# Kernel optimization log

Hardware: AMD Instinct MI355X
Metric: run time of the kernel (lower is better)

## Reference

```python
import jax, jax.numpy as jnp
import numpy as np

N_NODES = 50000
N_EDGES = 800000
IN_CH = 256
H1, D1 = 4, 64   # layer 1: 4 heads x 64 -> 256
H2, D2 = 1, 64   # output layer: 1 head x 64
NEG_SLOPE = 0.2  # DGL GATConv default


def _leaky_relu(x):
    return jnp.where(x >= 0, x, NEG_SLOPE * x)


def gat_conv(h, src, dst, W, attn_l, attn_r, bias, res_W, num_heads, out_feats, apply_elu):
    """DGL GATConv (eval mode, feat_drop=attn_drop=0).
    h: (N, F_in); src/dst: (E,) edge endpoints (edge u->v aggregates at v).
    W: (F_in, H*D); attn_l/attn_r: (H, D); bias: (H*D,); res_W: (F_in, H*D) or None.
    Returns (N, H, D).
    """
    N = h.shape[0]
    ft = (h @ W).reshape(N, num_heads, out_feats)            # (N,H,D)
    el = jnp.sum(ft * attn_l, axis=-1)                        # (N,H)
    er = jnp.sum(ft * attn_r, axis=-1)                        # (N,H)
    e = _leaky_relu(el[src] + er[dst])                        # (E,H)
    # segment softmax over incoming edges of each dst node
    emax = jax.ops.segment_max(e, dst, num_segments=N)        # (N,H)
    emax = jax.lax.stop_gradient(emax)
    ee = jnp.exp(e - emax[dst])                               # (E,H)
    denom = jax.ops.segment_sum(ee, dst, num_segments=N)      # (N,H)
    a = ee / denom[dst]                                       # (E,H)
    msg = ft[src] * a[:, :, None]                             # (E,H,D)
    rst = jax.ops.segment_sum(msg, dst, num_segments=N)       # (N,H,D)
    if res_W is not None:
        rst = rst + (h @ res_W).reshape(N, num_heads, out_feats)
    rst = rst + bias.reshape(num_heads, out_feats)
    if apply_elu:
        rst = jax.nn.elu(rst)
    return rst


def setup_inputs() -> dict:
    key = jax.random.key(0)
    ks = jax.random.split(key, 12)
    feat = jax.random.normal(ks[0], (N_NODES, IN_CH), dtype=jnp.float32)
    src = jax.random.randint(ks[1], (N_EDGES,), 0, N_NODES)
    dst = jax.random.randint(ks[2], (N_EDGES,), 0, N_NODES)
    s = 0.1
    W1 = jax.random.normal(ks[3], (IN_CH, H1 * D1), dtype=jnp.float32) * s
    al1 = jax.random.normal(ks[4], (H1, D1), dtype=jnp.float32) * s
    ar1 = jax.random.normal(ks[5], (H1, D1), dtype=jnp.float32) * s
    b1 = jnp.zeros((H1 * D1,), dtype=jnp.float32)
    W2 = jax.random.normal(ks[6], (H1 * D1, H2 * D2), dtype=jnp.float32) * s
    al2 = jax.random.normal(ks[7], (H2, D2), dtype=jnp.float32) * s
    ar2 = jax.random.normal(ks[8], (H2, D2), dtype=jnp.float32) * s
    b2 = jnp.zeros((H2 * D2,), dtype=jnp.float32)
    resW2 = jax.random.normal(ks[9], (H1 * D1, H2 * D2), dtype=jnp.float32) * s
    return {"feat": feat, "src": src, "dst": dst,
            "W1": W1, "al1": al1, "ar1": ar1, "b1": b1,
            "W2": W2, "al2": al2, "ar2": ar2, "b2": b2, "resW2": resW2}


def reference(feat, src, dst, W1, al1, ar1, b1, W2, al2, ar2, b2, resW2):
    # Layer 1: 4 heads, ELU, no residual (first DGL layer built without residual)
    h = gat_conv(feat, src, dst, W1, al1, ar1, b1, None, H1, D1, True)
    h = h.reshape(N_NODES, H1 * D1)  # flatten(1)
    # Layer 2: 1 head, residual (linear res_fc since 256 != 64), no activation
    h = gat_conv(h, src, dst, W2, al2, ar2, b2, resW2, H2, D2, False)
    return h.mean(axis=1)  # mean over output heads -> (N, out_channels)
```

## Files before the change

### kernel.cpp

```cpp
#include <hip/hip_runtime.h>
#include <math.h>

#define N_NODES 50000
#define N_EDGES 800000
#define ELL_W 64
#define CNT_STRIDE 16

#define E_SPLIT 400000
#define CONV_BLKS 1792
#define SCAT_BLKS 512

typedef __attribute__((ext_vector_type(8))) short bf16x8;
typedef __attribute__((ext_vector_type(4))) float f32x4;
typedef __attribute__((ext_vector_type(2))) float f32x2;

__device__ __forceinline__ float leaky(float x) { return x >= 0.f ? x : 0.2f * x; }
__device__ __forceinline__ unsigned short f2bf(float f) {
  unsigned u = __float_as_uint(f);
  return (unsigned short)((u + 0x7fffu + ((u >> 16) & 1u)) >> 16);
}
__device__ __forceinline__ float bflo(unsigned u) { return __uint_as_float(u << 16); }
__device__ __forceinline__ float bfhi(unsigned u) { return __uint_as_float(u & 0xffff0000u); }
__device__ __forceinline__ unsigned pack2(float a, float b) {
  return (unsigned)f2bf(a) | ((unsigned)f2bf(b) << 16);
}

__device__ __forceinline__ void scat4(const int* __restrict__ src, const int* __restrict__ dst,
                                      int* __restrict__ cnt, unsigned short* __restrict__ ell,
                                      int e) {
  int4 d4 = *(const int4*)(dst + e);
  int4 s4 = *(const int4*)(src + e);
  int sl;
  sl = atomicAdd(cnt + d4.x * CNT_STRIDE, 1);
  if (sl < ELL_W) __builtin_nontemporal_store((unsigned short)s4.x, ell + d4.x * ELL_W + sl);
  sl = atomicAdd(cnt + d4.y * CNT_STRIDE, 1);
  if (sl < ELL_W) __builtin_nontemporal_store((unsigned short)s4.y, ell + d4.y * ELL_W + sl);
  sl = atomicAdd(cnt + d4.z * CNT_STRIDE, 1);
  if (sl < ELL_W) __builtin_nontemporal_store((unsigned short)s4.z, ell + d4.z * ELL_W + sl);
  sl = atomicAdd(cnt + d4.w * CNT_STRIDE, 1);
  if (sl < ELL_W) __builtin_nontemporal_store((unsigned short)s4.w, ell + d4.w * ELL_W + sl);
}

__launch_bounds__(256)
__global__ void prep_k(const float* __restrict__ feat, const float* __restrict__ W1,
                       const float* __restrict__ W2, const float* __restrict__ resW2,
                       short* __restrict__ featb, short* __restrict__ Wt1,
                       short* __restrict__ Wt2, const int* __restrict__ src,
                       const int* __restrict__ dst, int* __restrict__ cnt,
                       unsigned short* __restrict__ ell) {
  if (blockIdx.x < SCAT_BLKS) {
    const int gtid = blockIdx.x * 256 + threadIdx.x;
    const int gsz = SCAT_BLKS * 256;
    for (int q = gtid; q < E_SPLIT / 4; q += gsz) scat4(src, dst, cnt, ell, q * 4);
    return;
  }
  const int gtid = (blockIdx.x - SCAT_BLKS) * 256 + threadIdx.x;
  const int gsz = CONV_BLKS * 256;
  for (int idx = gtid; idx < 256 * 256; idx += gsz) {
    int n = idx >> 8, k = idx & 255;
    Wt1[idx] = (short)f2bf(W1[(size_t)k * 256 + n]);
  }
  for (int idx = gtid; idx < 128 * 256; idx += gsz) {
    int n = idx >> 8, k = idx & 255;
    float v = (n < 64) ? W2[(size_t)k * 64 + n] : resW2[(size_t)k * 64 + (n - 64)];
    Wt2[idx] = (short)f2bf(v);
  }
  const float4* f4 = (const float4*)feat;
  uint2* fb2 = (uint2*)featb;
  for (int idx = gtid; idx < N_NODES * 64; idx += gsz) {
    float4 f = f4[idx];
    uint2 o;
    o.x = pack2(f.x, f.y);
    o.y = pack2(f.z, f.w);
    fb2[idx] = o;
  }
}

template <int MODE, bool SCAT>
__launch_bounds__(256)
__global__ void mfma_gemm_k(const short* __restrict__ A, const short* __restrict__ Bt,
                            const float* __restrict__ bias, const float* __restrict__ al,
                            const float* __restrict__ ar, float* __restrict__ elp,
                            float* __restrict__ erp, short* __restrict__ Cb,
                            float* __restrict__ Cf, const int* __restrict__ src,
                            const int* __restrict__ dst, int* __restrict__ cnt,
                            unsigned short* __restrict__ ell, int M, int K, int N) {
  constexpr int EPI_COLS = (MODE == 0) ? 136 : 72;
  union SharedU {
    struct { short As[4][128][8]; short Bs[4][128][8]; } ab;
    short epi[128 * EPI_COLS];
  };
  __shared__ SharedU sh;

  if (SCAT && blockIdx.y == 0) {
    const int gtid = blockIdx.x * 256 + threadIdx.x;
    const int gsz = gridDim.x * 256;
    for (int q = gtid; q < (N_EDGES - E_SPLIT) / 4; q += gsz)
      scat4(src, dst, cnt, ell, E_SPLIT + q * 4);
    return;
  }
  const int tid = threadIdx.x;
  const int bm0 = blockIdx.x * 128;
  const int bn0 = (SCAT ? ((int)blockIdx.y - 1) : (int)blockIdx.y) * 128;
  const int wave = tid >> 6, lane = tid & 63;
  const int wm = (wave & 1) * 64, wn = (wave >> 1) * 64;
  const int q = lane >> 4, r16 = lane & 15;
  const int srow = tid >> 1, sk = (tid & 1) * 16, sq = (tid & 1) * 2;
  f32x4 acc[4][4] = {};

  for (int k0 = 0; k0 < K; k0 += 32) {
    {
      uint4 v0 = {0, 0, 0, 0}, v1 = {0, 0, 0, 0};
      if (bm0 + srow < M) {
        const uint4* p = (const uint4*)(A + (size_t)(bm0 + srow) * K + k0 + sk);
        v0 = p[0];
        v1 = p[1];
      }
      *(uint4*)&sh.ab.As[sq][srow][0] = v0;
      *(uint4*)&sh.ab.As[sq + 1][srow][0] = v1;
    }
    {
      const uint4* p = (const uint4*)(Bt + (size_t)(bn0 + srow) * K + k0 + sk);
      *(uint4*)&sh.ab.Bs[sq][srow][0] = p[0];
      *(uint4*)&sh.ab.Bs[sq + 1][srow][0] = p[1];
    }
    __syncthreads();
    bf16x8 af[4], bfr[4];
#pragma unroll
    for (int i = 0; i < 4; ++i) af[i] = *(const bf16x8*)&sh.ab.As[q][wm + i * 16 + r16][0];
#pragma unroll
    for (int j = 0; j < 4; ++j) bfr[j] = *(const bf16x8*)&sh.ab.Bs[q][wn + j * 16 + r16][0];
#pragma unroll
    for (int i = 0; i < 4; ++i)
#pragma unroll
      for (int j = 0; j < 4; ++j)
        acc[i][j] = __builtin_amdgcn_mfma_f32_16x16x32_bf16(af[i], bfr[j], acc[i][j], 0, 0, 0);
    __syncthreads();
  }

  if (MODE == 0 || wn == 0) {
    const int head = (bn0 + wn) >> 6;
    float alv[4], arv[4];
#pragma unroll
    for (int j = 0; j < 4; ++j) {
      alv[j] = al[((MODE == 0) ? head * 64 : 0) + j * 16 + r16];
      arv[j] = ar[((MODE == 0) ? head * 64 : 0) + j * 16 + r16];
    }
#pragma unroll
    for (int i = 0; i < 4; ++i) {
#pragma unroll
      for (int reg = 0; reg < 4; ++reg) {
        float dl = acc[i][0][reg] * alv[0] + acc[i][1][reg] * alv[1] +
                   acc[i][2][reg] * alv[2] + acc[i][3][reg] * alv[3];
        float dr = acc[i][0][reg] * arv[0] + acc[i][1][reg] * arv[1] +
                   acc[i][2][reg] * arv[2] + acc[i][3][reg] * arv[3];
#pragma unroll
        for (int mm = 1; mm < 16; mm <<= 1) {
          dl += __shfl_xor(dl, mm);
          dr += __shfl_xor(dr, mm);
        }
        int row_g = bm0 + wm + i * 16 + q * 4 + reg;
        if (r16 == 0 && row_g < M) {
          if (MODE == 0) {
            elp[(size_t)row_g * 4 + head] = dl;
            erp[(size_t)row_g * 4 + head] = dr;
          } else {
            elp[row_g] = dl;
            erp[row_g] = dr;
          }
        }
      }
    }
  }

  if (MODE == 0) {
#pragma unroll
    for (int i = 0; i < 4; ++i)
#pragma unroll
      for (int reg = 0; reg < 4; ++reg) {
        int row = wm + i * 16 + q * 4 + reg;
#pragma unroll
        for (int j = 0; j < 4; ++j)
          sh.epi[row * EPI_COLS + wn + j * 16 + r16] = (short)f2bf(acc[i][j][reg]);
      }
    __syncthreads();
#pragma unroll
    for (int k = 0; k < 8; ++k) {
      int c = k * 256 + tid;
      int row = c >> 4, cc = c & 15;
      int row_g = bm0 + row;
      if (row_g < M) {
        uint4 v = *(const uint4*)&sh.epi[row * EPI_COLS + cc * 8];
        *(uint4*)(Cb + (size_t)row_g * N + bn0 + cc * 8) = v;
      }
    }
  } else {
    if (wn == 0) {
#pragma unroll
      for (int i = 0; i < 4; ++i)
#pragma unroll
        for (int reg = 0; reg < 4; ++reg) {
          int row = wm + i * 16 + q * 4 + reg;
#pragma unroll
          for (int j = 0; j < 4; ++j)
            sh.epi[row * EPI_COLS + j * 16 + r16] = (short)f2bf(acc[i][j][reg]);
        }
    } else {
#pragma unroll
      for (int i = 0; i < 4; ++i)
#pragma unroll
        for (int reg = 0; reg < 4; ++reg) {
          int row_g = bm0 + wm + i * 16 + q * 4 + reg;
          if (row_g >= M) continue;
#pragma unroll
          for (int j = 0; j < 4; ++j) {
            int col = j * 16 + r16;
            Cf[(size_t)row_g * 64 + col] = acc[i][j][reg] + bias[col];
          }
        }
    }
    __syncthreads();
#pragma unroll
    for (int k = 0; k < 4; ++k) {
      int c = k * 256 + tid;
      int row = c >> 3, cc = c & 7;
      int row_g = bm0 + row;
      if (row_g < M) {
        uint4 v = *(const uint4*)&sh.epi[row * EPI_COLS + cc * 8];
        *(uint4*)(Cb + (size_t)row_g * 64 + cc * 8) = v;
      }
    }
  }
}

__launch_bounds__(256)
__global__ void agg1_k(const unsigned short* __restrict__ ell, const int* __restrict__ cnt,
                       const float* __restrict__ el, const float* __restrict__ er,
                       const short* __restrict__ ft, const float* __restrict__ bias,
                       short* __restrict__ h1) {
  __shared__ unsigned wofs[4][64];
  __shared__ float wval[4][4][64];
  const int nib = threadIdx.x >> 6;
  const int node = blockIdx.x * 4 + nib;
  const int lane = threadIdx.x & 63;
  if (node >= N_NODES) return;
  const int deg = min(cnt[node * CNT_STRIDE], ELL_W);
  const unsigned short* row = ell + node * ELL_W;

  {
    int s_raw = row[lane];
    bool val = lane < deg;
    int s0 = deg > 0 ? (int)row[0] : 0;
    int s_safe = val ? s_raw : s0;
    float4 el4 = *(const float4*)(el + (size_t)s_safe * 4);
    float4 er4 = *(const float4*)(er + (size_t)node * 4);
    float w0 = val ? __expf(leaky(el4.x + er4.x)) : 0.f;
    float w1 = val ? __expf(leaky(el4.y + er4.y)) : 0.f;
    float w2 = val ? __expf(leaky(el4.z + er4.z)) : 0.f;
    float w3 = val ? __expf(leaky(el4.w + er4.w)) : 0.f;
    float d0 = w0, d1 = w1, d2 = w2, d3 = w3;
#pragma unroll
    for (int m = 1; m < 64; m <<= 1) {
      d0 += __shfl_xor(d0, m);
      d1 += __shfl_xor(d1, m);
      d2 += __shfl_xor(d2, m);
      d3 += __shfl_xor(d3, m);
    }
    float i0 = deg > 0 ? 1.f / d0 : 0.f;
    float i1 = deg > 0 ? 1.f / d1 : 0.f;
    float i2 = deg > 0 ? 1.f / d2 : 0.f;
    float i3 = deg > 0 ? 1.f / d3 : 0.f;
    wofs[nib][lane] = (unsigned)s_safe * 512u;
    wval[nib][0][lane] = w0 * i0;
    wval[nib][1][lane] = w1 * i1;
    wval[nib][2][lane] = w2 * i2;
    wval[nib][3][lane] = w3 * i3;
  }

  const int half = lane >> 5, l5 = lane & 31, h = l5 >> 3;
  const char* ftb = (const char*)ft + l5 * 16;
  const float* wv = &wval[nib][h][0];
  const unsigned* wo = &wofs[nib][0];
  f32x2 acc2[4] = {};
  const int degR = (deg + 7) & ~7;
  for (int i = 0; i < degR; i += 8) {
    unsigned o[4];
    float w[4];
    uint4 u[4];
#pragma unroll
    for (int k = 0; k < 4; ++k) {
      int slot = i + k * 2 + half;
      o[k] = wo[slot];
      w[k] = wv[slot];
    }
#pragma unroll
    for (int k = 0; k < 4; ++k) u[k] = *(const uint4*)(ftb + o[k]);
#pragma unroll
    for (int k = 0; k < 4; ++k) {
      f32x2 w2 = {w[k], w[k]};
      f32x2 p0 = {bflo(u[k].x), bfhi(u[k].x)};
      f32x2 p1 = {bflo(u[k].y), bfhi(u[k].y)};
      f32x2 p2 = {bflo(u[k].z), bfhi(u[k].z)};
      f32x2 p3 = {bflo(u[k].w), bfhi(u[k].w)};
      acc2[0] += w2 * p0;
      acc2[1] += w2 * p1;
      acc2[2] += w2 * p2;
      acc2[3] += w2 * p3;
    }
  }
#pragma unroll
  for (int j = 0; j < 4; ++j) {
    acc2[j][0] += __shfl_xor(acc2[j][0], 32);
    acc2[j][1] += __shfl_xor(acc2[j][1], 32);
  }
  if (half == 0) {
    float4 b0 = *(const float4*)(bias + l5 * 8);
    float4 b1 = *(const float4*)(bias + l5 * 8 + 4);
    float v[8];
    v[0] = acc2[0][0] + b0.x;
    v[1] = acc2[0][1] + b0.y;
    v[2] = acc2[1][0] + b0.z;
    v[3] = acc2[1][1] + b0.w;
    v[4] = acc2[2][0] + b1.x;
    v[5] = acc2[2][1] + b1.y;
    v[6] = acc2[3][0] + b1.z;
    v[7] = acc2[3][1] + b1.w;
#pragma unroll
    for (int k = 0; k < 8; ++k) v[k] = v[k] > 0.f ? v[k] : expm1f(v[k]);
    uint4 o;
    o.x = pack2(v[0], v[1]);
    o.y = pack2(v[2], v[3]);
    o.z = pack2(v[4], v[5]);
    o.w = pack2(v[6], v[7]);
    *(uint4*)(h1 + (size_t)node * 256 + l5 * 8) = o;
  }
}

__launch_bounds__(256)
__global__ void agg2_k(const unsigned short* __restrict__ ell, const int* __restrict__ cnt,
                       const float* __restrict__ el, const float* __restrict__ er,
                       const short* __restrict__ ft, float* __restrict__ out) {
  __shared__ uint2 wsl[4][64];
  const int nib = threadIdx.x >> 6;
  const int node = blockIdx.x * 4 + nib;
  const int lane = threadIdx.x & 63;
  if (node >= N_NODES) return;
  const int deg = min(cnt[node * CNT_STRIDE], ELL_W);
  const unsigned short* row = ell + node * ELL_W;

  {
    int s_raw = row[lane];
    bool val = lane < deg;
    int s0 = deg > 0 ? (int)row[0] : 0;
    int s_safe = val ? s_raw : s0;
    float erd = er[node];
    float w = val ? __expf(leaky(el[s_safe] + erd)) : 0.f;
    float d = w;
#pragma unroll
    for (int m = 1; m < 64; m <<= 1) d += __shfl_xor(d, m);
    float inv = deg > 0 ? 1.f / d : 0.f;
    uint2 e;
    e.x = (unsigned)s_safe * 128u;
    e.y = __float_as_uint(w * inv);
    wsl[nib][lane] = e;
  }

  const int qtr = lane >> 4, l4 = lane & 15;
  const char* ftb = (const char*)ft + l4 * 8;
  f32x2 acc2[2] = {};
  const int degR = (deg + 7) & ~7;
  for (int i = 0; i < degR; i += 8) {
#pragma unroll
    for (int k = 0; k < 2; ++k) {
      int slot = i + k * 4 + qtr;
      uint2 e = wsl[nib][slot];
      uint2 u = *(const uint2*)(ftb + e.x);
      float w = __uint_as_float(e.y);
      f32x2 w2 = {w, w};
      f32x2 p0 = {bflo(u.x), bfhi(u.x)};
      f32x2 p1 = {bflo(u.y), bfhi(u.y)};
      acc2[0] += w2 * p0;
      acc2[1] += w2 * p1;
    }
  }
#pragma unroll
  for (int j = 0; j < 2; ++j) {
#pragma unroll
    for (int c = 0; c < 2; ++c) {
      acc2[j][c] += __shfl_xor(acc2[j][c], 16);
      acc2[j][c] += __shfl_xor(acc2[j][c], 32);
    }
  }
  if (lane < 16) {
    float4* po = (float4*)(out + (size_t)node * 64 + l4 * 4);
    float4 o = *po;
    o.x += acc2[0][0];
    o.y += acc2[0][1];
    o.z += acc2[1][0];
    o.w += acc2[1][1];
    *po = o;
  }
}

extern "C" void kernel_launch(void* const* d_in, const int* in_sizes, int n_in,
                              void* d_out, int out_size, void* d_ws, size_t ws_size,
                              hipStream_t stream) {
  const float* feat  = (const float*)d_in[0];
  const int*   src   = (const int*)d_in[1];
  const int*   dst   = (const int*)d_in[2];
  const float* W1    = (const float*)d_in[3];
  const float* al1   = (const float*)d_in[4];
  const float* ar1   = (const float*)d_in[5];
  const float* b1    = (const float*)d_in[6];
  const float* W2    = (const float*)d_in[7];
  const float* al2   = (const float*)d_in[8];
  const float* ar2   = (const float*)d_in[9];
  const float* b2    = (const float*)d_in[10];
  const float* resW2 = (const float*)d_in[11];
  float* out = (float*)d_out;

  char* p = (char*)d_ws;
  short* featb = (short*)p; p += (size_t)N_NODES * 256 * 2;
  short* ft1b = (short*)p; p += (size_t)N_NODES * 256 * 2;
  short* h1b  = (short*)p; p += (size_t)N_NODES * 256 * 2;
  short* ft2b = (short*)p; p += (size_t)N_NODES * 64 * 2;
  short* Wt1  = (short*)p; p += 256 * 256 * 2;
  short* Wt2  = (short*)p; p += 128 * 256 * 2;
  float* el1  = (float*)p; p += (size_t)N_NODES * 4 * 4;
  float* er1  = (float*)p; p += (size_t)N_NODES * 4 * 4;
  float* el2  = (float*)p; p += (size_t)N_NODES * 4;
  float* er2  = (float*)p; p += (size_t)N_NODES * 4;
  int* cnt    = (int*)p;   p += (size_t)N_NODES * CNT_STRIDE * 4;
  unsigned short* ell = (unsigned short*)p; p += (size_t)N_NODES * ELL_W * 2;

  hipMemsetAsync(cnt, 0, (size_t)N_NODES * CNT_STRIDE * sizeof(int), stream);

  dim3 blk(256);

  prep_k<<<SCAT_BLKS + CONV_BLKS, blk, 0, stream>>>(feat, W1, W2, resW2, featb, Wt1, Wt2,
                                                    src, dst, cnt, ell);

  mfma_gemm_k<0, true><<<dim3(391, 3), blk, 0, stream>>>(
      featb, Wt1, nullptr, al1, ar1, el1, er1, ft1b, nullptr,
      src, dst, cnt, ell, N_NODES, 256, 256);
  agg1_k<<<12500, blk, 0, stream>>>(ell, cnt, el1, er1, ft1b, b1, h1b);

  mfma_gemm_k<1, false><<<dim3(391, 1), blk, 0, stream>>>(
      h1b, Wt2, b2, al2, ar2, el2, er2, ft2b, out,
      nullptr, nullptr, nullptr, nullptr, N_NODES, 256, 128);
  agg2_k<<<12500, blk, 0, stream>>>(ell, cnt, el2, er2, ft2b, out);
}
```

Before: 275.7 us.

## Process two nodes per wave in aggregation kernels and widen edge-scatter grid

Both aggregation kernels now assign two destination nodes to each wavefront, interleaving their gathers to raise memory-level parallelism and halving the grid. Layer-1 softmax weights and offsets are packed into one shared array so a single LDS read yields both. The scatter work inside the first GEMM now runs one item per thread over two grid rows, and the prep kernel block split is rebalanced. The cost is more registers per thread and wasted work when the two nodes' degrees differ.

```diff
diff --git a/kernel.cpp b/kernel.cpp
--- a/kernel.cpp
+++ b/kernel.cpp
@@ -7,8 +7,8 @@
 #define CNT_STRIDE 16
 
 #define E_SPLIT 400000
-#define CONV_BLKS 1792
-#define SCAT_BLKS 512
+#define CONV_BLKS 1024
+#define SCAT_BLKS 1024
 
 typedef __attribute__((ext_vector_type(8))) short bf16x8;
 typedef __attribute__((ext_vector_type(4))) float f32x4;
@@ -92,16 +92,14 @@
   };
   __shared__ SharedU sh;
 
-  if (SCAT && blockIdx.y == 0) {
-    const int gtid = blockIdx.x * 256 + threadIdx.x;
-    const int gsz = gridDim.x * 256;
-    for (int q = gtid; q < (N_EDGES - E_SPLIT) / 4; q += gsz)
-      scat4(src, dst, cnt, ell, E_SPLIT + q * 4);
+  if (SCAT && blockIdx.y < 2) {
+    const int gtid = (blockIdx.y * gridDim.x + blockIdx.x) * 256 + threadIdx.x;
+    if (gtid < (N_EDGES - E_SPLIT) / 4) scat4(src, dst, cnt, ell, E_SPLIT + gtid * 4);
     return;
   }
   const int tid = threadIdx.x;
   const int bm0 = blockIdx.x * 128;
-  const int bn0 = (SCAT ? ((int)blockIdx.y - 1) : (int)blockIdx.y) * 128;
+  const int bn0 = (SCAT ? ((int)blockIdx.y - 2) : (int)blockIdx.y) * 128;
   const int wave = tid >> 6, lane = tid & 63;
   const int wm = (wave & 1) * 64, wn = (wave >> 1) * 64;
   const int q = lane >> 4, r16 = lane & 15;
@@ -233,171 +231,209 @@
   }
 }
 
+#define AGG1_FMA(ACC, U, W)                     \
+  {                                             \
+    f32x2 w2_ = {(W), (W)};                     \
+    ACC[0] += w2_ * (f32x2){bflo((U).x), bfhi((U).x)}; \
+    ACC[1] += w2_ * (f32x2){bflo((U).y), bfhi((U).y)}; \
+    ACC[2] += w2_ * (f32x2){bflo((U).z), bfhi((U).z)}; \
+    ACC[3] += w2_ * (f32x2){bflo((U).w), bfhi((U).w)}; \
+  }
+
 __launch_bounds__(256)
 __global__ void agg1_k(const unsigned short* __restrict__ ell, const int* __restrict__ cnt,
                        const float* __restrict__ el, const float* __restrict__ er,
                        const short* __restrict__ ft, const float* __restrict__ bias,
                        short* __restrict__ h1) {
-  __shared__ unsigned wofs[4][64];
-  __shared__ float wval[4][4][64];
-  const int nib = threadIdx.x >> 6;
-  const int node = blockIdx.x * 4 + nib;
+  __shared__ uint2 wmeta[4][2][64][4];
+  const int wv = threadIdx.x >> 6;
   const int lane = threadIdx.x & 63;
-  if (node >= N_NODES) return;
-  const int deg = min(cnt[node * CNT_STRIDE], ELL_W);
-  const unsigned short* row = ell + node * ELL_W;
+  const int nodeA = blockIdx.x * 8 + wv * 2;
+  const int nodeB = nodeA + 1;
+  const int degA = min(cnt[nodeA * CNT_STRIDE], ELL_W);
+  const int degB = min(cnt[nodeB * CNT_STRIDE], ELL_W);
+  const unsigned short* rowA = ell + nodeA * ELL_W;
+  const unsigned short* rowB = ell + nodeB * ELL_W;
 
   {
-    int s_raw = row[lane];
-    bool val = lane < deg;
-    int s0 = deg > 0 ? (int)row[0] : 0;
-    int s_safe = val ? s_raw : s0;
-    float4 el4 = *(const float4*)(el + (size_t)s_safe * 4);
-    float4 er4 = *(const float4*)(er + (size_t)node * 4);
-    float w0 = val ? __expf(leaky(el4.x + er4.x)) : 0.f;
-    float w1 = val ? __expf(leaky(el4.y + er4.y)) : 0.f;
-    float w2 = val ? __expf(leaky(el4.z + er4.z)) : 0.f;
-    float w3 = val ? __expf(leaky(el4.w + er4.w)) : 0.f;
-    float d0 = w0, d1 = w1, d2 = w2, d3 = w3;
+    int sA = lane < degA ? (int)rowA[lane] : (degA > 0 ? (int)rowA[0] : 0);
+    int sB = lane < degB ? (int)rowB[lane] : (degB > 0 ? (int)rowB[0] : 0);
+    float4 elA = *(const float4*)(el + (size_t)sA * 4);
+    float4 elB = *(const float4*)(el + (size_t)sB * 4);
+    float4 erA = *(const float4*)(er + (size_t)nodeA * 4);
+    float4 erB = *(const float4*)(er + (size_t)nodeB * 4);
+    float a0 = lane < degA ? __expf(leaky(elA.x + erA.x)) : 0.f;
+    float a1 = lane < degA ? __expf(leaky(elA.y + erA.y)) : 0.f;
+    float a2 = lane < degA ? __expf(leaky(elA.z + erA.z)) : 0.f;
+    float a3 = lane < degA ? __expf(leaky(elA.w + erA.w)) : 0.f;
+    float b0 = lane < degB ? __expf(leaky(elB.x + erB.x)) : 0.f;
+    float b1 = lane < degB ? __expf(leaky(elB.y + erB.y)) : 0.f;
+    float b2 = lane < degB ? __expf(leaky(elB.z + erB.z)) : 0.f;
+    float b3 = lane < degB ? __expf(leaky(elB.w + erB.w)) : 0.f;
+    float dA0 = a0, dA1 = a1, dA2 = a2, dA3 = a3;
+    float dB0 = b0, dB1 = b1, dB2 = b2, dB3 = b3;
 #pragma unroll
     for (int m = 1; m < 64; m <<= 1) {
-      d0 += __shfl_xor(d0, m);
-      d1 += __shfl_xor(d1, m);
-      d2 += __shfl_xor(d2, m);
-      d3 += __shfl_xor(d3, m);
-    }
-    float i0 = deg > 0 ? 1.f / d0 : 0.f;
-    float i1 = deg > 0 ? 1.f / d1 : 0.f;
-    float i2 = deg > 0 ? 1.f / d2 : 0.f;
-    float i3 = deg > 0 ? 1.f / d3 : 0.f;
-    wofs[nib][lane] = (unsigned)s_safe * 512u;
-    wval[nib][0][lane] = w0 * i0;
-    wval[nib][1][lane] = w1 * i1;
-    wval[nib][2][lane] = w2 * i2;
-    wval[nib][3][lane] = w3 * i3;
+      dA0 += __shfl_xor(dA0, m);
+      dB0 += __shfl_xor(dB0, m);
+      dA1 += __shfl_xor(dA1, m);
+      dB1 += __shfl_xor(dB1, m);
+      dA2 += __shfl_xor(dA2, m);
+      dB2 += __shfl_xor(dB2, m);
+      dA3 += __shfl_xor(dA3, m);
+      dB3 += __shfl_xor(dB3, m);
+    }
+    unsigned ofA = (unsigned)sA * 512u, ofB = (unsigned)sB * 512u;
+    uint4 pa0, pa1, pb0, pb1;
+    pa0.x = ofA; pa0.y = __float_as_uint(degA > 0 ? a0 / dA0 : 0.f);
+    pa0.z = ofA; pa0.w = __float_as_uint(degA > 0 ? a1 / dA1 : 0.f);
+    pa1.x = ofA; pa1.y = __float_as_uint(degA > 0 ? a2 / dA2 : 0.f);
+    pa1.z = ofA; pa1.w = __float_as_uint(degA > 0 ? a3 / dA3 : 0.f);
+    pb0.x = ofB; pb0.y = __float_as_uint(degB > 0 ? b0 / dB0 : 0.f);
+    pb0.z = ofB; pb0.w = __float_as_uint(degB > 0 ? b1 / dB1 : 0.f);
+    pb1.x = ofB; pb1.y = __float_as_uint(degB > 0 ? b2 / dB2 : 0.f);
+    pb1.z = ofB; pb1.w = __float_as_uint(degB > 0 ? b3 / dB3 : 0.f);
+    *(uint4*)&wmeta[wv][0][lane][0] = pa0;
+    *(uint4*)&wmeta[wv][0][lane][2] = pa1;
+    *(uint4*)&wmeta[wv][1][lane][0] = pb0;
+    *(uint4*)&wmeta[wv][1][lane][2] = pb1;
   }
 
   const int half = lane >> 5, l5 = lane & 31, h = l5 >> 3;
   const char* ftb = (const char*)ft + l5 * 16;
-  const float* wv = &wval[nib][h][0];
-  const unsigned* wo = &wofs[nib][0];
-  f32x2 acc2[4] = {};
-  const int degR = (deg + 7) & ~7;
-  for (int i = 0; i < degR; i += 8) {
-    unsigned o[4];
-    float w[4];
-    uint4 u[4];
+  f32x2 accA[4] = {}, accB[4] = {};
+  const int degM = max((degA + 7) & ~7, (degB + 7) & ~7);
+  for (int i = 0; i < degM; i += 8) {
+    unsigned oA[4], oB[4];
+    float wA[4], wB[4];
 #pragma unroll
     for (int k = 0; k < 4; ++k) {
-      int slot = i + k * 2 + half;
-      o[k] = wo[slot];
-      w[k] = wv[slot];
-    }
-#pragma unroll
-    for (int k = 0; k < 4; ++k) u[k] = *(const uint4*)(ftb + o[k]);
+      uint2 mA = wmeta[wv][0][i + k * 2 + half][h];
+      uint2 mB = wmeta[wv][1][i + k * 2 + half][h];
+      oA[k] = mA.x;
+      wA[k] = __uint_as_float(mA.y);
+      oB[k] = mB.x;
+      wB[k] = __uint_as_float(mB.y);
+    }
+    uint4 uA[4], uB[4];
 #pragma unroll
     for (int k = 0; k < 4; ++k) {
-      f32x2 w2 = {w[k], w[k]};
-      f32x2 p0 = {bflo(u[k].x), bfhi(u[k].x)};
-      f32x2 p1 = {bflo(u[k].y), bfhi(u[k].y)};
-      f32x2 p2 = {bflo(u[k].z), bfhi(u[k].z)};
-      f32x2 p3 = {bflo(u[k].w), bfhi(u[k].w)};
-      acc2[0] += w2 * p0;
-      acc2[1] += w2 * p1;
-      acc2[2] += w2 * p2;
-      acc2[3] += w2 * p3;
-    }
-  }
+      uA[k] = *(const uint4*)(ftb + oA[k]);
+      uB[k] = *(const uint4*)(ftb + oB[k]);
+    }
+#pragma unroll
+    for (int k = 0; k < 4; ++k) {
+      AGG1_FMA(accA, uA[k], wA[k]);
+      AGG1_FMA(accB, uB[k], wB[k]);
+    }
+  }
+
 #pragma unroll
   for (int j = 0; j < 4; ++j) {
-    acc2[j][0] += __shfl_xor(acc2[j][0], 32);
-    acc2[j][1] += __shfl_xor(acc2[j][1], 32);
-  }
-  if (half == 0) {
-    float4 b0 = *(const float4*)(bias + l5 * 8);
-    float4 b1 = *(const float4*)(bias + l5 * 8 + 4);
-    float v[8];
-    v[0] = acc2[0][0] + b0.x;
-    v[1] = acc2[0][1] + b0.y;
-    v[2] = acc2[1][0] + b0.z;
-    v[3] = acc2[1][1] + b0.w;
-    v[4] = acc2[2][0] + b1.x;
-    v[5] = acc2[2][1] + b1.y;
-    v[6] = acc2[3][0] + b1.z;
-    v[7] = acc2[3][1] + b1.w;
-#pragma unroll
-    for (int k = 0; k < 8; ++k) v[k] = v[k] > 0.f ? v[k] : expm1f(v[k]);
-    uint4 o;
-    o.x = pack2(v[0], v[1]);
-    o.y = pack2(v[2], v[3]);
-    o.z = pack2(v[4], v[5]);
-    o.w = pack2(v[6], v[7]);
-    *(uint4*)(h1 + (size_t)node * 256 + l5 * 8) = o;
-  }
+    accA[j][0] += __shfl_xor(accA[j][0], 32);
+    accA[j][1] += __shfl_xor(accA[j][1], 32);
+    accB[j][0] += __shfl_xor(accB[j][0], 32);
+    accB[j][1] += __shfl_xor(accB[j][1], 32);
+  }
+  const int node = half ? nodeB : nodeA;
+  float v[8];
+#pragma unroll
+  for (int j = 0; j < 4; ++j) {
+    v[2 * j] = half ? accB[j][0] : accA[j][0];
+    v[2 * j + 1] = half ? accB[j][1] : accA[j][1];
+  }
+  float4 b0 = *(const float4*)(bias + l5 * 8);
+  float4 b1 = *(const float4*)(bias + l5 * 8 + 4);
+  v[0] += b0.x; v[1] += b0.y; v[2] += b0.z; v[3] += b0.w;
+  v[4] += b1.x; v[5] += b1.y; v[6] += b1.z; v[7] += b1.w;
+#pragma unroll
+  for (int k = 0; k < 8; ++k) v[k] = v[k] > 0.f ? v[k] : expm1f(v[k]);
+  uint4 o;
+  o.x = pack2(v[0], v[1]);
+  o.y = pack2(v[2], v[3]);
+  o.z = pack2(v[4], v[5]);
+  o.w = pack2(v[6], v[7]);
+  *(uint4*)(h1 + (size_t)node * 256 + l5 * 8) = o;
 }
 
 __launch_bounds__(256)
 __global__ void agg2_k(const unsigned short* __restrict__ ell, const int* __restrict__ cnt,
                        const float* __restrict__ el, const float* __restrict__ er,
                        const short* __restrict__ ft, float* __restrict__ out) {
-  __shared__ uint2 wsl[4][64];
-  const int nib = threadIdx.x >> 6;
-  const int node = blockIdx.x * 4 + nib;
+  __shared__ uint2 wsl[4][2][64];
+  const int wv = threadIdx.x >> 6;
   const int lane = threadIdx.x & 63;
-  if (node >= N_NODES) return;
-  const int deg = min(cnt[node * CNT_STRIDE], ELL_W);
-  const unsigned short* row = ell + node * ELL_W;
+  const int nodeA = blockIdx.x * 8 + wv * 2;
+  const int nodeB = nodeA + 1;
+  const int degA = min(cnt[nodeA * CNT_STRIDE], ELL_W);
+  const int degB = min(cnt[nodeB * CNT_STRIDE], ELL_W);
+  const unsigned short* rowA = ell + nodeA * ELL_W;
+  const unsigned short* rowB = ell + nodeB * ELL_W;
 
   {
-    int s_raw = row[lane];
-    bool val = lane < deg;
-    int s0 = deg > 0 ? (int)row[0] : 0;
-    int s_safe = val ? s_raw : s0;
-    float erd = er[node];
-    float w = val ? __expf(leaky(el[s_safe] + erd)) : 0.f;
-    float d = w;
-#pragma unroll
-    for (int m = 1; m < 64; m <<= 1) d += __shfl_xor(d, m);
-    float inv = deg > 0 ? 1.f / d : 0.f;
-    uint2 e;
-    e.x = (unsigned)s_safe * 128u;
-    e.y = __float_as_uint(w * inv);
-    wsl[nib][lane] = e;
+    int sA = lane < degA ? (int)rowA[lane] : (degA > 0 ? (int)rowA[0] : 0);
+    int sB = lane < degB ? (int)rowB[lane] : (degB > 0 ? (int)rowB[0] : 0);
+    float wa = lane < degA ? __expf(leaky(el[sA] + er[nodeA])) : 0.f;
+    float wb = lane < degB ? __expf(leaky(el[sB] + er[nodeB])) : 0.f;
+    float da = wa, db = wb;
+#pragma unroll
+    for (int m = 1; m < 64; m <<= 1) {
+      da += __shfl_xor(da, m);
+      db += __shfl_xor(db, m);
+    }
+    uint2 ea, eb;
+    ea.x = (unsigned)sA * 128u;
+    ea.y = __float_as_uint(degA > 0 ? wa / da : 0.f);
+    eb.x = (unsigned)sB * 128u;
+    eb.y = __float_as_uint(degB > 0 ? wb / db : 0.f);
+    wsl[wv][0][lane] = ea;
+    wsl[wv][1][lane] = eb;
   }
 
   const int qtr = lane >> 4, l4 = lane & 15;
   const char* ftb = (const char*)ft + l4 * 8;
-  f32x2 acc2[2] = {};
-  const int degR = (deg + 7) & ~7;
-  for (int i = 0; i < degR; i += 8) {
+  f32x2 accA[2] = {}, accB[2] = {};
+  const int degM = max((degA + 7) & ~7, (degB + 7) & ~7);
+  for (int i = 0; i < degM; i += 8) {
 #pragma unroll
     for (int k = 0; k < 2; ++k) {
       int slot = i + k * 4 + qtr;
-      uint2 e = wsl[nib][slot];
-      uint2 u = *(const uint2*)(ftb + e.x);
-      float w = __uint_as_float(e.y);
-      f32x2 w2 = {w, w};
-      f32x2 p0 = {bflo(u.x), bfhi(u.x)};
-      f32x2 p1 = {bflo(u.y), bfhi(u.y)};
-      acc2[0] += w2 * p0;
-      acc2[1] += w2 * p1;
+      uint2 ea = wsl[wv][0][slot];
+      uint2 eb = wsl[wv][1][slot];
+      uint2 ua = *(const uint2*)(ftb + ea.x);
+      uint2 ub = *(const uint2*)(ftb + eb.x);
+      float wa = __uint_as_float(ea.y);
+      float wb = __uint_as_float(eb.y);
+      f32x2 wa2 = {wa, wa}, wb2 = {wb, wb};
+      accA[0] += wa2 * (f32x2){bflo(ua.x), bfhi(ua.x)};
+      accA[1] += wa2 * (f32x2){bflo(ua.y), bfhi(ua.y)};
+      accB[0] += wb2 * (f32x2){bflo(ub.x), bfhi(ub.x)};
+      accB[1] += wb2 * (f32x2){bflo(ub.y), bfhi(ub.y)};
     }
   }
 #pragma unroll
   for (int j = 0; j < 2; ++j) {
 #pragma unroll
     for (int c = 0; c < 2; ++c) {
-      acc2[j][c] += __shfl_xor(acc2[j][c], 16);
-      acc2[j][c] += __shfl_xor(acc2[j][c], 32);
-    }
-  }
-  if (lane < 16) {
+      accA[j][c] += __shfl_xor(accA[j][c], 16);
+      accA[j][c] += __shfl_xor(accA[j][c], 32);
+      accB[j][c] += __shfl_xor(accB[j][c], 16);
+      accB[j][c] += __shfl_xor(accB[j][c], 32);
+    }
+  }
+  if (lane < 32) {
+    const int node = lane < 16 ? nodeA : nodeB;
+    float4 add;
+    add.x = lane < 16 ? accA[0][0] : accB[0][0];
+    add.y = lane < 16 ? accA[0][1] : accB[0][1];
+    add.z = lane < 16 ? accA[1][0] : accB[1][0];
+    add.w = lane < 16 ? accA[1][1] : accB[1][1];
     float4* po = (float4*)(out + (size_t)node * 64 + l4 * 4);
     float4 o = *po;
-    o.x += acc2[0][0];
-    o.y += acc2[0][1];
-    o.z += acc2[1][0];
-    o.w += acc2[1][1];
+    o.x += add.x;
+    o.y += add.y;
+    o.z += add.z;
+    o.w += add.w;
     *po = o;
   }
 }
@@ -440,13 +476,13 @@
   prep_k<<<SCAT_BLKS + CONV_BLKS, blk, 0, stream>>>(feat, W1, W2, resW2, featb, Wt1, Wt2,
                                                     src, dst, cnt, ell);
 
-  mfma_gemm_k<0, true><<<dim3(391, 3), blk, 0, stream>>>(
+  mfma_gemm_k<0, true><<<dim3(391, 4), blk, 0, stream>>>(
       featb, Wt1, nullptr, al1, ar1, el1, er1, ft1b, nullptr,
       src, dst, cnt, ell, N_NODES, 256, 256);
-  agg1_k<<<12500, blk, 0, stream>>>(ell, cnt, el1, er1, ft1b, b1, h1b);
+  agg1_k<<<6250, blk, 0, stream>>>(ell, cnt, el1, er1, ft1b, b1, h1b);
 
   mfma_gemm_k<1, false><<<dim3(391, 1), blk, 0, stream>>>(
       h1b, Wt2, b2, al2, ar2, el2, er2, ft2b, out,
       nullptr, nullptr, nullptr, nullptr, N_NODES, 256, 128);
-  agg2_k<<<12500, blk, 0, stream>>>(ell, cnt, el2, er2, ft2b, out);
-}
+  agg2_k<<<6250, blk, 0, stream>>>(ell, cnt, el2, er2, ft2b, out);
+}
```

After: 274.4 us. No clear change (-0.5%).
